# Kernel optimization log

Measured on AMD Instinct MI355X. Metric: run time of the kernel, lower is better.

The kernel has to match this reference:

```python
import jax, jax.numpy as jnp
import numpy as np

H = 256          # h_dim
SEQ_LEN = 10     # max history length
B = 2048         # number of queries with non-empty history
N = 327680       # total flattened neighbors across all (query, timestep) segments
NUM_SEG = B * SEQ_LEN
NUM_ENT = 20000
NUM_REL = 200


def setup_inputs() -> dict:
    key = jax.random.key(0)
    ks = jax.random.split(key, 9)
    s = jax.random.randint(ks[0], (B,), 0, NUM_ENT)
    r = jax.random.randint(ks[1], (B,), 0, NUM_REL)
    nbr_ids = jax.random.randint(ks[2], (N,), 0, NUM_ENT)
    seg_ids = jnp.sort(jax.random.randint(ks[3], (N,), 0, NUM_SEG))
    ent_embeds = jax.random.normal(ks[4], (NUM_ENT, H), dtype=jnp.float32)
    rel_embeds = jax.random.normal(ks[5], (NUM_REL, H), dtype=jnp.float32)
    W_attn = jax.random.normal(ks[6], (3 * H, H), dtype=jnp.float32) * 0.05
    b_attn = jax.random.normal(ks[7], (H,), dtype=jnp.float32) * 0.05
    v_s = jax.random.normal(ks[8], (H, 1), dtype=jnp.float32) * 0.05
    return {"s": s, "r": r, "nbr_ids": nbr_ids, "seg_ids": seg_ids,
            "ent_embeds": ent_embeds, "rel_embeds": rel_embeds,
            "W_attn": W_attn, "b_attn": b_attn, "v_s": v_s}


def reference(s, r, nbr_ids, seg_ids, ent_embeds, rel_embeds, W_attn, b_attn, v_s):
    # Per-neighbor gathers. Each neighbor belongs to segment seg = q*SEQ_LEN + t.
    q = seg_ids // SEQ_LEN                              # query index per neighbor [N]
    em = ent_embeds[nbr_ids]                            # [N, H] neighbor embeddings
    s_emb = ent_embeds[s]                               # [B, H]
    r_emb = rel_embeds[r]                               # [B, H]
    ss = s_emb[q]                                       # [N, H]
    rr = r_emb[q]                                       # [N, H]
    # Score: tanh(Linear(3H -> H)) @ v_s  -> scalar per neighbor
    x = jnp.concatenate([em, ss, rr], axis=1)           # [N, 3H]
    scores = (jnp.tanh(x @ W_attn + b_attn) @ v_s)[:, 0]  # [N]
    # Segment softmax over neighbors within each (query, timestep) segment.
    m = jax.ops.segment_max(scores, seg_ids, num_segments=NUM_SEG)  # [S]
    e = jnp.exp(scores - m[seg_ids])                    # [N]
    denom = jax.ops.segment_sum(e, seg_ids, num_segments=NUM_SEG)   # [S]
    w = e / denom[seg_ids]                              # [N]
    # Weighted sum of neighbor embeddings per segment (scatter-reduce).
    agg = jax.ops.segment_sum(w[:, None] * em, seg_ids, num_segments=NUM_SEG)  # [S, H]
    counts = jax.ops.segment_sum(jnp.ones_like(scores), seg_ids, num_segments=NUM_SEG)
    mask = (counts > 0).astype(em.dtype).reshape(B, SEQ_LEN, 1)     # present timesteps
    agg = agg.reshape(B, SEQ_LEN, H)
    ss_t = jnp.broadcast_to(s_emb[:, None, :], (B, SEQ_LEN, H))
    rr_t = jnp.broadcast_to(r_emb[:, None, :], (B, SEQ_LEN, H))
    # Padded [B, SEQ_LEN, 3H] sequence tensor (rows for empty segments are zero,
    # matching the torch code's zero-initialized padded tensor). Dropout p=0.0.
    out = jnp.concatenate([agg, ss_t, rr_t], axis=2) * mask
    return out
```

## Files before the change

### kernel.cpp

```cpp
#include <hip/hip_runtime.h>
#include <hip/hip_bf16.h>

#define H 256
#define SEQ 10

typedef __attribute__((ext_vector_type(8))) short bf16x8;
typedef __attribute__((ext_vector_type(4))) short bf16x4;
typedef __attribute__((ext_vector_type(4))) float f32x4;

__device__ __forceinline__ unsigned short f2bf(float x) {
    union { float f; unsigned u; } v; v.f = x;
    unsigned r = v.u + 0x7fff + ((v.u >> 16) & 1);
    return (unsigned short)(r >> 16);
}
__device__ __forceinline__ float bf2f(unsigned short b) {
    union { unsigned u; float f; } v; v.u = ((unsigned)b) << 16;
    return v.f;
}
__device__ __forceinline__ float fexp2(float x) {
    return __builtin_amdgcn_exp2f(x);
}
__device__ __forceinline__ float fast_tanh(float x) {
    float t = fexp2(x * 2.885390082f);
    return 1.f - 2.f * __builtin_amdgcn_rcpf(t + 1.f);
}

__global__ void prep_Wt_kernel(const float* __restrict__ W,
                               unsigned short* __restrict__ Wt) {
    int idx = blockIdx.x * blockDim.x + threadIdx.x;
    if (idx >= H * 3 * H) return;
    int n = idx / (3 * H), k = idx % (3 * H);
    Wt[idx] = f2bf(W[k * H + n]);
}

__global__ void seg_start_kernel(const int* __restrict__ seg_ids,
                                 int* __restrict__ seg_start, int n, int num_seg) {
    int j = blockIdx.x * blockDim.x + threadIdx.x;
    if (j >= n) return;
    int cur = seg_ids[j];
    int prev = (j == 0) ? -1 : seg_ids[j - 1];
    for (int s2 = prev + 1; s2 <= cur; s2++) seg_start[s2] = j;
    if (j == n - 1)
        for (int s2 = cur + 1; s2 <= num_seg; s2++) seg_start[s2] = n;
}

__global__ void gemm_bf16_kernel(const float* __restrict__ entf,
                                 const int* __restrict__ sidx,
                                 const int* __restrict__ ridx,
                                 const float* __restrict__ ent,
                                 const float* __restrict__ rel,
                                 const unsigned short* __restrict__ Wt,
                                 const float* __restrict__ bias,
                                 unsigned short* __restrict__ out,
                                 unsigned short* __restrict__ em_out,
                                 int M, int K, int k0, int mode, int ldo) {
    __shared__ unsigned short As[64][40];
    __shared__ unsigned short Bs[64][40];
    int t = threadIdx.x;
    int m0 = blockIdx.x * 64;
    int n0 = blockIdx.y * 64;
    int sr = t >> 2;
    int sc = (t & 3) * 8;
    int wave = t >> 6, lane = t & 63;
    int lr = lane & 15, lg = lane >> 4;

    f32x4 acc[4] = {{0.f, 0.f, 0.f, 0.f}, {0.f, 0.f, 0.f, 0.f},
                    {0.f, 0.f, 0.f, 0.f}, {0.f, 0.f, 0.f, 0.f}};

    for (int kk = 0; kk < K; kk += 32) {
        bf16x8 av = {};
        int gm = m0 + sr;
        if (gm < M) {
            const float* src;
            if (mode == 0) {
                src = entf + (size_t)gm * H + kk + sc;
            } else {
                int k = kk + sc;
                src = (k < H) ? (ent + (size_t)sidx[gm] * H + k)
                              : (rel + (size_t)ridx[gm] * H + (k - H));
            }
            float4 f0 = *reinterpret_cast<const float4*>(src);
            float4 f1 = *reinterpret_cast<const float4*>(src + 4);
            av[0] = (short)f2bf(f0.x); av[1] = (short)f2bf(f0.y);
            av[2] = (short)f2bf(f0.z); av[3] = (short)f2bf(f0.w);
            av[4] = (short)f2bf(f1.x); av[5] = (short)f2bf(f1.y);
            av[6] = (short)f2bf(f1.z); av[7] = (short)f2bf(f1.w);
            if (mode == 0 && em_out && n0 == 0)
                *reinterpret_cast<bf16x8*>(em_out + (size_t)gm * 512 + 256 + kk + sc) = av;
        }
        *reinterpret_cast<bf16x8*>(&As[sr][sc]) = av;
        bf16x8 bv = *reinterpret_cast<const bf16x8*>(
            Wt + (size_t)(n0 + sr) * (3 * H) + k0 + kk + sc);
        *reinterpret_cast<bf16x8*>(&Bs[sr][sc]) = bv;
        __syncthreads();

        bf16x8 bfr = *reinterpret_cast<const bf16x8*>(&Bs[wave * 16 + lr][lg * 8]);
#pragma unroll
        for (int mf = 0; mf < 4; mf++) {
            bf16x8 afr = *reinterpret_cast<const bf16x8*>(&As[mf * 16 + lr][lg * 8]);
            acc[mf] = __builtin_amdgcn_mfma_f32_16x16x32_bf16(afr, bfr, acc[mf], 0, 0, 0);
        }
        __syncthreads();
    }

    int col = n0 + wave * 16 + lr;
    float bv = bias ? bias[col] : 0.f;
#pragma unroll
    for (int mf = 0; mf < 4; mf++) {
#pragma unroll
        for (int rr = 0; rr < 4; rr++) {
            int row = m0 + mf * 16 + lg * 4 + rr;
            if (row < M)
                out[(size_t)row * ldo + col] = f2bf(acc[mf][rr] + bv);
        }
    }
}

__global__ void __launch_bounds__(128)
fused_agg_kernel(const int* __restrict__ nbr_ids,
                 const int* __restrict__ seg_start,
                 const unsigned short* __restrict__ comb,
                 const unsigned short* __restrict__ qpartbf,
                 const float* __restrict__ v_s,
                 const float* __restrict__ ent_embeds,
                 const float* __restrict__ rel_embeds,
                 const int* __restrict__ s,
                 const int* __restrict__ r,
                 float* __restrict__ out, int num_seg) {
    int seg = blockIdx.x * 2 + (threadIdx.x >> 6);
    if (seg >= num_seg) return;
    int lane = threadIdx.x & 63;
    int b = seg / SEQ;
    int start = seg_start[seg], end = seg_start[seg + 1];
    float* orow = out + (size_t)seg * (3 * H);
    int c4 = lane * 4;

    if (start == end) {
        float4 z = {0.f, 0.f, 0.f, 0.f};
        *reinterpret_cast<float4*>(orow + c4) = z;
        *reinterpret_cast<float4*>(orow + H + c4) = z;
        *reinterpret_cast<float4*>(orow + 2 * H + c4) = z;
        return;
    }

    int g = lane >> 4, li = lane & 15;
    int cb = li * 16;

    float qv[16], vv[16];
    {
        bf16x8 qa = *reinterpret_cast<const bf16x8*>(qpartbf + (size_t)b * H + cb);
        bf16x8 qb = *reinterpret_cast<const bf16x8*>(qpartbf + (size_t)b * H + cb + 8);
#pragma unroll
        for (int k = 0; k < 8; k++) {
            qv[k] = bf2f((unsigned short)qa[k]);
            qv[8 + k] = bf2f((unsigned short)qb[k]);
        }
        const float4* vp = reinterpret_cast<const float4*>(v_s + cb);
#pragma unroll
        for (int k = 0; k < 4; k++) {
            float4 tv = vp[k];
            vv[4 * k + 0] = tv.x; vv[4 * k + 1] = tv.y;
            vv[4 * k + 2] = tv.z; vv[4 * k + 3] = tv.w;
        }
    }

    float acc[16];
#pragma unroll
    for (int k = 0; k < 16; k++) acc[k] = 0.f;
    float lpart = 0.f;

    int cc = end - start;
    int nitm = (cc + 3) >> 2;

    int j0 = min(g, cc - 1);
    const unsigned short* row = comb + (size_t)nbr_ids[start + j0] * 512 + cb;
    bf16x8 p0 = *reinterpret_cast<const bf16x8*>(row);
    bf16x8 p1 = *reinterpret_cast<const bf16x8*>(row + 8);
    bf16x8 e0 = *reinterpret_cast<const bf16x8*>(row + 256);
    bf16x8 e1 = *reinterpret_cast<const bf16x8*>(row + 264);

    for (int ji = 0; ji < nitm; ji++) {
        int jn = min(4 * (ji + 1) + g, cc - 1);
        const unsigned short* rown = comb + (size_t)nbr_ids[start + jn] * 512 + cb;
        bf16x8 p0n = *reinterpret_cast<const bf16x8*>(rown);
        bf16x8 p1n = *reinterpret_cast<const bf16x8*>(rown + 8);
        bf16x8 e0n = *reinterpret_cast<const bf16x8*>(rown + 256);
        bf16x8 e1n = *reinterpret_cast<const bf16x8*>(rown + 264);

        float s16 = 0.f;
#pragma unroll
        for (int k = 0; k < 8; k++) {
            s16 += fast_tanh(bf2f((unsigned short)p0[k]) + qv[k]) * vv[k];
            s16 += fast_tanh(bf2f((unsigned short)p1[k]) + qv[8 + k]) * vv[8 + k];
        }
        s16 += __shfl_xor(s16, 1);
        s16 += __shfl_xor(s16, 2);
        s16 += __shfl_xor(s16, 4);
        s16 += __shfl_xor(s16, 8);
        float e = fexp2(s16 * 1.4426950408889634f);
        e = (4 * ji + g < cc) ? e : 0.f;
        lpart += e;
#pragma unroll
        for (int k = 0; k < 8; k++) {
            acc[k] += e * bf2f((unsigned short)e0[k]);
            acc[8 + k] += e * bf2f((unsigned short)e1[k]);
        }
        p0 = p0n; p1 = p1n; e0 = e0n; e1 = e1n;
    }

    lpart += __shfl_xor(lpart, 16);
    lpart += __shfl_xor(lpart, 32);
#pragma unroll
    for (int k = 0; k < 16; k++) {
        acc[k] += __shfl_xor(acc[k], 16);
        acc[k] += __shfl_xor(acc[k], 32);
    }
    float invl = 1.f / lpart;

    float4 o;
#pragma unroll
    for (int k = 0; k < 4; k++) {
        float v0 = acc[k], v1 = acc[4 + k], v2 = acc[8 + k], v3 = acc[12 + k];
        float pick = (g == 0) ? v0 : (g == 1) ? v1 : (g == 2) ? v2 : v3;
        if (k == 0) o.x = pick * invl;
        else if (k == 1) o.y = pick * invl;
        else if (k == 2) o.z = pick * invl;
        else o.w = pick * invl;
    }
    *reinterpret_cast<float4*>(orow + cb + 4 * g) = o;
    *reinterpret_cast<float4*>(orow + H + c4) =
        *reinterpret_cast<const float4*>(ent_embeds + (size_t)s[b] * H + c4);
    *reinterpret_cast<float4*>(orow + 2 * H + c4) =
        *reinterpret_cast<const float4*>(rel_embeds + (size_t)r[b] * H + c4);
}

extern "C" void kernel_launch(void* const* d_in, const int* in_sizes, int n_in,
                              void* d_out, int out_size, void* d_ws, size_t ws_size,
                              hipStream_t stream) {
    const int* s = (const int*)d_in[0];
    const int* r = (const int*)d_in[1];
    const int* nbr_ids = (const int*)d_in[2];
    const int* seg_ids = (const int*)d_in[3];
    const float* ent_embeds = (const float*)d_in[4];
    const float* rel_embeds = (const float*)d_in[5];
    const float* W_attn = (const float*)d_in[6];
    const float* b_attn = (const float*)d_in[7];
    const float* v_s = (const float*)d_in[8];
    float* out = (float*)d_out;

    int B = in_sizes[0];
    int N = in_sizes[2];
    int num_ent = in_sizes[4] / H;
    int num_seg = B * SEQ;

    char* ws = (char*)d_ws;
    unsigned short* comb = (unsigned short*)ws;
    unsigned short* Wt = comb + (size_t)num_ent * 512;
    unsigned short* qpartbf = Wt + (size_t)H * 3 * H;
    int* seg_start = (int*)(qpartbf + (size_t)B * H);

    prep_Wt_kernel<<<(H * 3 * H + 255) / 256, 256, 0, stream>>>(W_attn, Wt);
    seg_start_kernel<<<(N + 255) / 256, 256, 0, stream>>>(seg_ids, seg_start, N, num_seg);

    dim3 g1((num_ent + 63) / 64, H / 64);
    gemm_bf16_kernel<<<g1, 256, 0, stream>>>(ent_embeds, nullptr, nullptr, nullptr, nullptr,
                                             Wt, nullptr, comb, comb,
                                             num_ent, H, 0, 0, 512);
    dim3 g2(B / 64, H / 64);
    gemm_bf16_kernel<<<g2, 256, 0, stream>>>(nullptr, s, r, ent_embeds, rel_embeds,
                                             Wt, b_attn, qpartbf, nullptr,
                                             B, 2 * H, H, 1, H);

    fused_agg_kernel<<<(num_seg + 1) / 2, 128, 0, stream>>>(
        nbr_ids, seg_start, comb, qpartbf, v_s,
        ent_embeds, rel_embeds, s, r, out, num_seg);
}
```

Before: 103.9 us.

## Fuse prep kernels, widen GEMM N-tile, persistent agg waves, fold tanh constants

Merges the weight-transpose and segment-start kernels into one launch. Widens each GEMM block to cover all 256 output columns, so ent_embeds rows are loaded and converted once instead of four times. The 2*log2(e) factor is folded into W and the bias, and tanh·v is rewritten as vsum - 2·v·rcp(exp2+1), which removes a multiply and a subtract per element. The aggregation kernel becomes a fixed-grid loop where each wave handles a contiguous chunk of segments and reuses the query vector across segments of the same batch, at the cost of possible load imbalance and more register pressure.

```diff
diff --git a/kernel.cpp b/kernel.cpp
--- a/kernel.cpp
+++ b/kernel.cpp
@@ -3,9 +3,10 @@
 
 #define H 256
 #define SEQ 10
+#define C2LOG2E 2.8853900817779268f
+#define LOG2E 1.4426950408889634f
 
 typedef __attribute__((ext_vector_type(8))) short bf16x8;
-typedef __attribute__((ext_vector_type(4))) short bf16x4;
 typedef __attribute__((ext_vector_type(4))) float f32x4;
 
 __device__ __forceinline__ unsigned short f2bf(float x) {
@@ -20,28 +21,26 @@
 __device__ __forceinline__ float fexp2(float x) {
     return __builtin_amdgcn_exp2f(x);
 }
-__device__ __forceinline__ float fast_tanh(float x) {
-    float t = fexp2(x * 2.885390082f);
-    return 1.f - 2.f * __builtin_amdgcn_rcpf(t + 1.f);
-}
-
-__global__ void prep_Wt_kernel(const float* __restrict__ W,
-                               unsigned short* __restrict__ Wt) {
-    int idx = blockIdx.x * blockDim.x + threadIdx.x;
-    if (idx >= H * 3 * H) return;
-    int n = idx / (3 * H), k = idx % (3 * H);
-    Wt[idx] = f2bf(W[k * H + n]);
-}
-
-__global__ void seg_start_kernel(const int* __restrict__ seg_ids,
-                                 int* __restrict__ seg_start, int n, int num_seg) {
-    int j = blockIdx.x * blockDim.x + threadIdx.x;
-    if (j >= n) return;
-    int cur = seg_ids[j];
-    int prev = (j == 0) ? -1 : seg_ids[j - 1];
-    for (int s2 = prev + 1; s2 <= cur; s2++) seg_start[s2] = j;
-    if (j == n - 1)
-        for (int s2 = cur + 1; s2 <= num_seg; s2++) seg_start[s2] = n;
+
+__global__ void prep_kernel(const float* __restrict__ W,
+                            unsigned short* __restrict__ Wt,
+                            const int* __restrict__ seg_ids,
+                            int* __restrict__ seg_start,
+                            int nWt, int n, int num_seg) {
+    if ((int)blockIdx.x < nWt) {
+        int idx = blockIdx.x * 256 + threadIdx.x;
+        if (idx >= H * 3 * H) return;
+        int nn = idx / (3 * H), k = idx % (3 * H);
+        Wt[idx] = f2bf(C2LOG2E * W[k * H + nn]);
+    } else {
+        int j = (blockIdx.x - nWt) * 256 + threadIdx.x;
+        if (j >= n) return;
+        int cur = seg_ids[j];
+        int prev = (j == 0) ? -1 : seg_ids[j - 1];
+        for (int s2 = prev + 1; s2 <= cur; s2++) seg_start[s2] = j;
+        if (j == n - 1)
+            for (int s2 = cur + 1; s2 <= num_seg; s2++) seg_start[s2] = n;
+    }
 }
 
 __global__ void gemm_bf16_kernel(const float* __restrict__ entf,
@@ -55,17 +54,19 @@
                                  unsigned short* __restrict__ em_out,
                                  int M, int K, int k0, int mode, int ldo) {
     __shared__ unsigned short As[64][40];
-    __shared__ unsigned short Bs[64][40];
+    __shared__ unsigned short Bs[256][40];
     int t = threadIdx.x;
     int m0 = blockIdx.x * 64;
-    int n0 = blockIdx.y * 64;
     int sr = t >> 2;
     int sc = (t & 3) * 8;
     int wave = t >> 6, lane = t & 63;
     int lr = lane & 15, lg = lane >> 4;
 
-    f32x4 acc[4] = {{0.f, 0.f, 0.f, 0.f}, {0.f, 0.f, 0.f, 0.f},
-                    {0.f, 0.f, 0.f, 0.f}, {0.f, 0.f, 0.f, 0.f}};
+    f32x4 acc[4][4];
+#pragma unroll
+    for (int i = 0; i < 4; i++)
+#pragma unroll
+        for (int jn = 0; jn < 4; jn++) acc[i][jn] = (f32x4){0.f, 0.f, 0.f, 0.f};
 
     for (int kk = 0; kk < K; kk += 32) {
         bf16x8 av = {};
@@ -85,38 +86,52 @@
             av[2] = (short)f2bf(f0.z); av[3] = (short)f2bf(f0.w);
             av[4] = (short)f2bf(f1.x); av[5] = (short)f2bf(f1.y);
             av[6] = (short)f2bf(f1.z); av[7] = (short)f2bf(f1.w);
-            if (mode == 0 && em_out && n0 == 0)
+            if (mode == 0 && em_out)
                 *reinterpret_cast<bf16x8*>(em_out + (size_t)gm * 512 + 256 + kk + sc) = av;
         }
         *reinterpret_cast<bf16x8*>(&As[sr][sc]) = av;
-        bf16x8 bv = *reinterpret_cast<const bf16x8*>(
-            Wt + (size_t)(n0 + sr) * (3 * H) + k0 + kk + sc);
-        *reinterpret_cast<bf16x8*>(&Bs[sr][sc]) = bv;
+#pragma unroll
+        for (int r4 = 0; r4 < 4; r4++) {
+            int row = r4 * 64 + sr;
+            bf16x8 bv = *reinterpret_cast<const bf16x8*>(
+                Wt + (size_t)row * (3 * H) + k0 + kk + sc);
+            *reinterpret_cast<bf16x8*>(&Bs[row][sc]) = bv;
+        }
         __syncthreads();
 
-        bf16x8 bfr = *reinterpret_cast<const bf16x8*>(&Bs[wave * 16 + lr][lg * 8]);
-#pragma unroll
-        for (int mf = 0; mf < 4; mf++) {
-            bf16x8 afr = *reinterpret_cast<const bf16x8*>(&As[mf * 16 + lr][lg * 8]);
-            acc[mf] = __builtin_amdgcn_mfma_f32_16x16x32_bf16(afr, bfr, acc[mf], 0, 0, 0);
-        }
+        bf16x8 afr[4], bfr[4];
+#pragma unroll
+        for (int am = 0; am < 4; am++)
+            afr[am] = *reinterpret_cast<const bf16x8*>(&As[am * 16 + lr][lg * 8]);
+#pragma unroll
+        for (int bn = 0; bn < 4; bn++)
+            bfr[bn] = *reinterpret_cast<const bf16x8*>(&Bs[wave * 64 + bn * 16 + lr][lg * 8]);
+#pragma unroll
+        for (int am = 0; am < 4; am++)
+#pragma unroll
+            for (int bn = 0; bn < 4; bn++)
+                acc[am][bn] = __builtin_amdgcn_mfma_f32_16x16x32_bf16(
+                    afr[am], bfr[bn], acc[am][bn], 0, 0, 0);
         __syncthreads();
     }
 
-    int col = n0 + wave * 16 + lr;
-    float bv = bias ? bias[col] : 0.f;
-#pragma unroll
-    for (int mf = 0; mf < 4; mf++) {
-#pragma unroll
-        for (int rr = 0; rr < 4; rr++) {
-            int row = m0 + mf * 16 + lg * 4 + rr;
-            if (row < M)
-                out[(size_t)row * ldo + col] = f2bf(acc[mf][rr] + bv);
-        }
-    }
-}
-
-__global__ void __launch_bounds__(128)
+#pragma unroll
+    for (int bn = 0; bn < 4; bn++) {
+        int col = wave * 64 + bn * 16 + lr;
+        float bv = bias ? C2LOG2E * bias[col] : 0.f;
+#pragma unroll
+        for (int am = 0; am < 4; am++) {
+#pragma unroll
+            for (int rr = 0; rr < 4; rr++) {
+                int row = m0 + am * 16 + lg * 4 + rr;
+                if (row < M)
+                    out[(size_t)row * ldo + col] = f2bf(acc[am][bn][rr] + bv);
+            }
+        }
+    }
+}
+
+__global__ void __launch_bounds__(128, 4)
 fused_agg_kernel(const int* __restrict__ nbr_ids,
                  const int* __restrict__ seg_start,
                  const unsigned short* __restrict__ comb,
@@ -127,111 +142,129 @@
                  const int* __restrict__ s,
                  const int* __restrict__ r,
                  float* __restrict__ out, int num_seg) {
-    int seg = blockIdx.x * 2 + (threadIdx.x >> 6);
-    if (seg >= num_seg) return;
+    int wid = blockIdx.x * 2 + (threadIdx.x >> 6);
+    int nw = gridDim.x * 2;
     int lane = threadIdx.x & 63;
-    int b = seg / SEQ;
-    int start = seg_start[seg], end = seg_start[seg + 1];
-    float* orow = out + (size_t)seg * (3 * H);
-    int c4 = lane * 4;
-
-    if (start == end) {
-        float4 z = {0.f, 0.f, 0.f, 0.f};
-        *reinterpret_cast<float4*>(orow + c4) = z;
-        *reinterpret_cast<float4*>(orow + H + c4) = z;
-        *reinterpret_cast<float4*>(orow + 2 * H + c4) = z;
-        return;
-    }
-
     int g = lane >> 4, li = lane & 15;
     int cb = li * 16;
-
-    float qv[16], vv[16];
+    int c4 = lane * 4;
+
+    int chunk = (num_seg + nw - 1) / nw;
+    int sbeg = wid * chunk;
+    int send = min(sbeg + chunk, num_seg);
+
+    float vm2[16];
+    float vsum = 0.f;
     {
-        bf16x8 qa = *reinterpret_cast<const bf16x8*>(qpartbf + (size_t)b * H + cb);
-        bf16x8 qb = *reinterpret_cast<const bf16x8*>(qpartbf + (size_t)b * H + cb + 8);
-#pragma unroll
-        for (int k = 0; k < 8; k++) {
-            qv[k] = bf2f((unsigned short)qa[k]);
-            qv[8 + k] = bf2f((unsigned short)qb[k]);
-        }
         const float4* vp = reinterpret_cast<const float4*>(v_s + cb);
 #pragma unroll
         for (int k = 0; k < 4; k++) {
             float4 tv = vp[k];
-            vv[4 * k + 0] = tv.x; vv[4 * k + 1] = tv.y;
-            vv[4 * k + 2] = tv.z; vv[4 * k + 3] = tv.w;
-        }
-    }
-
-    float acc[16];
-#pragma unroll
-    for (int k = 0; k < 16; k++) acc[k] = 0.f;
-    float lpart = 0.f;
-
-    int cc = end - start;
-    int nitm = (cc + 3) >> 2;
-
-    int j0 = min(g, cc - 1);
-    const unsigned short* row = comb + (size_t)nbr_ids[start + j0] * 512 + cb;
-    bf16x8 p0 = *reinterpret_cast<const bf16x8*>(row);
-    bf16x8 p1 = *reinterpret_cast<const bf16x8*>(row + 8);
-    bf16x8 e0 = *reinterpret_cast<const bf16x8*>(row + 256);
-    bf16x8 e1 = *reinterpret_cast<const bf16x8*>(row + 264);
-
-    for (int ji = 0; ji < nitm; ji++) {
-        int jn = min(4 * (ji + 1) + g, cc - 1);
-        const unsigned short* rown = comb + (size_t)nbr_ids[start + jn] * 512 + cb;
-        bf16x8 p0n = *reinterpret_cast<const bf16x8*>(rown);
-        bf16x8 p1n = *reinterpret_cast<const bf16x8*>(rown + 8);
-        bf16x8 e0n = *reinterpret_cast<const bf16x8*>(rown + 256);
-        bf16x8 e1n = *reinterpret_cast<const bf16x8*>(rown + 264);
-
-        float s16 = 0.f;
-#pragma unroll
-        for (int k = 0; k < 8; k++) {
-            s16 += fast_tanh(bf2f((unsigned short)p0[k]) + qv[k]) * vv[k];
-            s16 += fast_tanh(bf2f((unsigned short)p1[k]) + qv[8 + k]) * vv[8 + k];
-        }
-        s16 += __shfl_xor(s16, 1);
-        s16 += __shfl_xor(s16, 2);
-        s16 += __shfl_xor(s16, 4);
-        s16 += __shfl_xor(s16, 8);
-        float e = fexp2(s16 * 1.4426950408889634f);
-        e = (4 * ji + g < cc) ? e : 0.f;
-        lpart += e;
-#pragma unroll
-        for (int k = 0; k < 8; k++) {
-            acc[k] += e * bf2f((unsigned short)e0[k]);
-            acc[8 + k] += e * bf2f((unsigned short)e1[k]);
-        }
-        p0 = p0n; p1 = p1n; e0 = e0n; e1 = e1n;
-    }
-
-    lpart += __shfl_xor(lpart, 16);
-    lpart += __shfl_xor(lpart, 32);
-#pragma unroll
-    for (int k = 0; k < 16; k++) {
-        acc[k] += __shfl_xor(acc[k], 16);
-        acc[k] += __shfl_xor(acc[k], 32);
-    }
-    float invl = 1.f / lpart;
-
-    float4 o;
-#pragma unroll
-    for (int k = 0; k < 4; k++) {
-        float v0 = acc[k], v1 = acc[4 + k], v2 = acc[8 + k], v3 = acc[12 + k];
-        float pick = (g == 0) ? v0 : (g == 1) ? v1 : (g == 2) ? v2 : v3;
-        if (k == 0) o.x = pick * invl;
-        else if (k == 1) o.y = pick * invl;
-        else if (k == 2) o.z = pick * invl;
-        else o.w = pick * invl;
-    }
-    *reinterpret_cast<float4*>(orow + cb + 4 * g) = o;
-    *reinterpret_cast<float4*>(orow + H + c4) =
-        *reinterpret_cast<const float4*>(ent_embeds + (size_t)s[b] * H + c4);
-    *reinterpret_cast<float4*>(orow + 2 * H + c4) =
-        *reinterpret_cast<const float4*>(rel_embeds + (size_t)r[b] * H + c4);
+            vm2[4 * k + 0] = -2.f * tv.x; vm2[4 * k + 1] = -2.f * tv.y;
+            vm2[4 * k + 2] = -2.f * tv.z; vm2[4 * k + 3] = -2.f * tv.w;
+            vsum += tv.x + tv.y + tv.z + tv.w;
+        }
+    }
+
+    float qv[16];
+    int bcur = -1;
+
+    for (int seg = sbeg; seg < send; seg++) {
+        int start = seg_start[seg], end = seg_start[seg + 1];
+        int b = seg / SEQ;
+        float* orow = out + (size_t)seg * (3 * H);
+
+        if (start == end) {
+            float4 z = {0.f, 0.f, 0.f, 0.f};
+            *reinterpret_cast<float4*>(orow + c4) = z;
+            *reinterpret_cast<float4*>(orow + H + c4) = z;
+            *reinterpret_cast<float4*>(orow + 2 * H + c4) = z;
+            continue;
+        }
+
+        if (b != bcur) {
+            bcur = b;
+            bf16x8 qa = *reinterpret_cast<const bf16x8*>(qpartbf + (size_t)b * H + cb);
+            bf16x8 qb = *reinterpret_cast<const bf16x8*>(qpartbf + (size_t)b * H + cb + 8);
+#pragma unroll
+            for (int k = 0; k < 8; k++) {
+                qv[k] = bf2f((unsigned short)qa[k]);
+                qv[8 + k] = bf2f((unsigned short)qb[k]);
+            }
+        }
+
+        float acc[16];
+#pragma unroll
+        for (int k = 0; k < 16; k++) acc[k] = 0.f;
+        float lpart = 0.f;
+
+        int cc = end - start;
+        int nitm = (cc + 3) >> 2;
+
+        int j0 = min(g, cc - 1);
+        const unsigned short* row = comb + (size_t)nbr_ids[start + j0] * 512 + cb;
+        bf16x8 p0 = *reinterpret_cast<const bf16x8*>(row);
+        bf16x8 p1 = *reinterpret_cast<const bf16x8*>(row + 8);
+
+        for (int ji = 0; ji < nitm; ji++) {
+            bf16x8 e0 = *reinterpret_cast<const bf16x8*>(row + 256);
+            bf16x8 e1 = *reinterpret_cast<const bf16x8*>(row + 264);
+            int jn = min(4 * (ji + 1) + g, cc - 1);
+            const unsigned short* rown = comb + (size_t)nbr_ids[start + jn] * 512 + cb;
+            bf16x8 p0n = *reinterpret_cast<const bf16x8*>(rown);
+            bf16x8 p1n = *reinterpret_cast<const bf16x8*>(rown + 8);
+
+            float s16 = 0.f;
+#pragma unroll
+            for (int k = 0; k < 8; k++) {
+                float r0 = __builtin_amdgcn_rcpf(
+                    fexp2(bf2f((unsigned short)p0[k]) + qv[k]) + 1.f);
+                s16 = fmaf(vm2[k], r0, s16);
+                float r1 = __builtin_amdgcn_rcpf(
+                    fexp2(bf2f((unsigned short)p1[k]) + qv[8 + k]) + 1.f);
+                s16 = fmaf(vm2[8 + k], r1, s16);
+            }
+            s16 += vsum;
+            s16 += __shfl_xor(s16, 1);
+            s16 += __shfl_xor(s16, 2);
+            s16 += __shfl_xor(s16, 4);
+            s16 += __shfl_xor(s16, 8);
+            float e = fexp2(s16 * LOG2E);
+            e = (4 * ji + g < cc) ? e : 0.f;
+            lpart += e;
+#pragma unroll
+            for (int k = 0; k < 8; k++) {
+                acc[k] = fmaf(e, bf2f((unsigned short)e0[k]), acc[k]);
+                acc[8 + k] = fmaf(e, bf2f((unsigned short)e1[k]), acc[8 + k]);
+            }
+            p0 = p0n; p1 = p1n; row = rown;
+        }
+
+        lpart += __shfl_xor(lpart, 16);
+        lpart += __shfl_xor(lpart, 32);
+#pragma unroll
+        for (int k = 0; k < 16; k++) {
+            acc[k] += __shfl_xor(acc[k], 16);
+            acc[k] += __shfl_xor(acc[k], 32);
+        }
+        float invl = 1.f / lpart;
+
+        float4 o;
+#pragma unroll
+        for (int k = 0; k < 4; k++) {
+            float v0 = acc[k], v1 = acc[4 + k], v2 = acc[8 + k], v3 = acc[12 + k];
+            float pick = (g == 0) ? v0 : (g == 1) ? v1 : (g == 2) ? v2 : v3;
+            if (k == 0) o.x = pick * invl;
+            else if (k == 1) o.y = pick * invl;
+            else if (k == 2) o.z = pick * invl;
+            else o.w = pick * invl;
+        }
+        *reinterpret_cast<float4*>(orow + cb + 4 * g) = o;
+        *reinterpret_cast<float4*>(orow + H + c4) =
+            *reinterpret_cast<const float4*>(ent_embeds + (size_t)s[b] * H + c4);
+        *reinterpret_cast<float4*>(orow + 2 * H + c4) =
+            *reinterpret_cast<const float4*>(rel_embeds + (size_t)r[b] * H + c4);
+    }
 }
 
 extern "C" void kernel_launch(void* const* d_in, const int* in_sizes, int n_in,
@@ -259,19 +292,19 @@
     unsigned short* qpartbf = Wt + (size_t)H * 3 * H;
     int* seg_start = (int*)(qpartbf + (size_t)B * H);
 
-    prep_Wt_kernel<<<(H * 3 * H + 255) / 256, 256, 0, stream>>>(W_attn, Wt);
-    seg_start_kernel<<<(N + 255) / 256, 256, 0, stream>>>(seg_ids, seg_start, N, num_seg);
-
-    dim3 g1((num_ent + 63) / 64, H / 64);
-    gemm_bf16_kernel<<<g1, 256, 0, stream>>>(ent_embeds, nullptr, nullptr, nullptr, nullptr,
-                                             Wt, nullptr, comb, comb,
-                                             num_ent, H, 0, 0, 512);
-    dim3 g2(B / 64, H / 64);
-    gemm_bf16_kernel<<<g2, 256, 0, stream>>>(nullptr, s, r, ent_embeds, rel_embeds,
-                                             Wt, b_attn, qpartbf, nullptr,
-                                             B, 2 * H, H, 1, H);
-
-    fused_agg_kernel<<<(num_seg + 1) / 2, 128, 0, stream>>>(
+    int nWt = (H * 3 * H + 255) / 256;
+    int nSeg = (N + 255) / 256;
+    prep_kernel<<<nWt + nSeg, 256, 0, stream>>>(W_attn, Wt, seg_ids, seg_start,
+                                                nWt, N, num_seg);
+
+    gemm_bf16_kernel<<<(num_ent + 63) / 64, 256, 0, stream>>>(
+        ent_embeds, nullptr, nullptr, nullptr, nullptr,
+        Wt, nullptr, comb, comb, num_ent, H, 0, 0, 512);
+    gemm_bf16_kernel<<<B / 64, 256, 0, stream>>>(
+        nullptr, s, r, ent_embeds, rel_embeds,
+        Wt, b_attn, qpartbf, nullptr, B, 2 * H, H, 1, H);
+
+    fused_agg_kernel<<<2048, 128, 0, stream>>>(
         nbr_ids, seg_start, comb, qpartbf, v_s,
         ent_embeds, rel_embeds, s, r, out, num_seg);
 }
```

Result: no change. 106.0 us (+2.0%).
